# Kernel optimization log

Measured on AMD Instinct MI355X. Metric: run time of the kernel, lower is better.

The kernel has to match this reference:

```python
import jax, jax.numpy as jnp
import numpy as np

HEADS = 8
DIM_HEAD = 64


def setup_inputs() -> dict:
    key = jax.random.key(0)
    ks = jax.random.split(key, 5)
    B, N, C, coor = 2, 2048, 256, 3
    dim_inner = HEADS * DIM_HEAD  # 512
    # weight scale 1/16 ~ 1/sqrt(256) keeps softmax logits in a sane range
    w_scale = 1.0 / 16.0
    return {
        "x": jax.random.normal(ks[0], (B, N, C, coor), dtype=jnp.float32),
        "Wq": jax.random.normal(ks[1], (dim_inner, C), dtype=jnp.float32) * w_scale,
        "Wk": jax.random.normal(ks[2], (dim_inner, C), dtype=jnp.float32) * w_scale,
        "Wv": jax.random.normal(ks[3], (dim_inner, C), dtype=jnp.float32) * w_scale,
        "Wo": jax.random.normal(ks[4], (C, dim_inner), dtype=jnp.float32) * w_scale,
    }


def _split_heads(t, B, N, coor):
    # b n (h d) c -> b h n (d c)
    t = t.reshape(B, N, HEADS, DIM_HEAD, coor)
    t = t.transpose(0, 2, 1, 3, 4)
    return t.reshape(B, HEADS, N, DIM_HEAD * coor)


def reference(x, Wq, Wk, Wv, Wo):
    B, N, C, coor = x.shape
    # VNLinear: einsum('... i c, o i -> ... o c')
    q = jnp.einsum('bnic,oi->bnoc', x, Wq)
    k = jnp.einsum('bnic,oi->bnoc', x, Wk)
    v = jnp.einsum('bnic,oi->bnoc', x, Wv)
    q = _split_heads(q, B, N, coor)  # (B, H, N, d*c)
    k = _split_heads(k, B, N, coor)
    v = _split_heads(v, B, N, coor)
    scale = (DIM_HEAD * coor) ** -0.5
    sim = jnp.einsum('bhie,bhje->bhij', q, k) * scale  # (B, H, N, N)
    attn = jax.nn.softmax(sim, axis=-1)
    out = jnp.einsum('bhij,bhje->bhie', attn, v)  # (B, H, N, d*c)
    # b h n (d c) -> b n (h d) c
    out = out.reshape(B, HEADS, N, DIM_HEAD, coor).transpose(0, 2, 1, 3, 4)
    out = out.reshape(B, N, HEADS * DIM_HEAD, coor)
    # to_out VNLinear
    return jnp.einsum('bnic,oi->bnoc', out, Wo)  # (B, N, C, 3)
```

## Files before the change

kernel.cpp:

```cpp
#include <hip/hip_runtime.h>

#define HEADS 8
#define DH 64
#define CO 3
#define E 192
#define NSEQ 2048
#define BATCH 2
#define CIN 256
#define DINNER 512
#define NTOK 4096
#define BHTOT 16

typedef __attribute__((ext_vector_type(8))) short bf16x8;
typedef __attribute__((ext_vector_type(4))) short bf16x4;
typedef __attribute__((ext_vector_type(4))) float f32x4;

static __device__ inline short f2bf(float f) {
  union { float f; unsigned u; } v; v.f = f;
  unsigned r = (v.u + 0x7FFFu + ((v.u >> 16) & 1u)) >> 16;
  return (short)r;
}

static __device__ inline void load_lds16(const short* g, short* l) {
  __builtin_amdgcn_global_load_lds(
      (const __attribute__((address_space(1))) void*)g,
      (__attribute__((address_space(3))) void*)l, 16, 0, 0);
}


__global__ __launch_bounds__(256) void prep_w(const float* __restrict__ Wq,
                                              const float* __restrict__ Wk,
                                              const float* __restrict__ Wv,
                                              const float* __restrict__ Wo,
                                              short* __restrict__ wqkvp,
                                              short* __restrict__ wop) {
  int idx = blockIdx.x * 256 + threadIdx.x;
  const float qscale = 0.07216878364870323f * 1.4426950408889634f;
  if (idx < 1536 * 256) {
    int o = idx >> 8, i = idx & 255;
    float v;
    if (o < 512) v = Wq[idx] * qscale;
    else if (o < 1024) v = Wk[idx - 512 * 256];
    else v = Wv[idx - 1024 * 256];
    int nt = o >> 4, ln = o & 15, ks = i >> 5, qd = (i >> 3) & 3, j = i & 7;
    wqkvp[((size_t)(nt * 8 + ks)) * 512 + (qd * 16 + ln) * 8 + j] = f2bf(v);
  } else {
    int j0 = idx - 1536 * 256;
    if (j0 < 256 * 512) {
      int o2 = j0 >> 9, i = j0 & 511;
      int nt = o2 >> 4, ln = o2 & 15, ks = i >> 5, qd = (i >> 3) & 3, j = i & 7;
      wop[((size_t)(nt * 16 + ks)) * 512 + (qd * 16 + ln) * 8 + j] = f2bf(Wo[j0]);
    }
  }
}

__global__ __launch_bounds__(256) void prep_x(const float* __restrict__ x,
                                              short* __restrict__ xcp) {
  int idx = blockIdx.x * 256 + threadIdx.x;
  int t = idx >> 8, i = idx & 255;
  const float* p = x + (size_t)idx * 3;
  float a = p[0], b = p[1], c = p[2];
  int mt = t >> 4, ln = t & 15, ks = i >> 5, qd = (i >> 3) & 3, j = i & 7;
  size_t inner = (size_t)(qd * 16 + ln) * 8 + j;
  xcp[((size_t)(0 * 256 + mt) * 8 + ks) * 512 + inner] = f2bf(a);
  xcp[((size_t)(1 * 256 + mt) * 8 + ks) * 512 + inner] = f2bf(b);
  xcp[((size_t)(2 * 256 + mt) * 8 + ks) * 512 + inner] = f2bf(c);
}

__global__ __launch_bounds__(256) void qkv_gemm(const short* __restrict__ xcp,
                                                const short* __restrict__ wqkvp,
                                                short* __restrict__ qp,
                                                short* __restrict__ kp,
                                                short* __restrict__ vp) {
  __shared__ __align__(16) short pool[17408];
  int c = blockIdx.z, ntb = blockIdx.x, mtb = blockIdx.y;
  int tid = threadIdx.x, wave = tid >> 6, lane = tid & 63;
  int ln = lane & 15, quad = lane >> 4;
  int wm = wave >> 1, wn = wave & 1;

  const short* gA = xcp + ((size_t)(c * 256 + mtb * 8) * 8) * 512;
  const short* gB = wqkvp + ((size_t)(ntb * 8) * 8) * 512;

  f32x4 acc[4][4] = {};
#pragma unroll
  for (int i = 0; i < 2; i++) {
    int q = tid + 256 * i, mf = q >> 6, l = q & 63;
    load_lds16(gA + (size_t)(mf * 8) * 512 + l * 8, pool + q * 8);
    load_lds16(gB + (size_t)(mf * 8) * 512 + l * 8, pool + 8192 + q * 8);
  }
  for (int ks = 0; ks < 8; ks++) {
    int b = ks & 1;
    __syncthreads();
    if (ks < 7) {
#pragma unroll
      for (int i = 0; i < 2; i++) {
        int q = tid + 256 * i, mf = q >> 6, l = q & 63;
        load_lds16(gA + (size_t)(mf * 8 + ks + 1) * 512 + l * 8, pool + (b ^ 1) * 4096 + q * 8);
        load_lds16(gB + (size_t)(mf * 8 + ks + 1) * 512 + l * 8, pool + 8192 + (b ^ 1) * 4096 + q * 8);
      }
    }
    const short* As = pool + b * 4096;
    const short* Bs = pool + 8192 + b * 4096;
    bf16x8 af[4], bfr[4];
#pragma unroll
    for (int i = 0; i < 4; i++) af[i] = *(const bf16x8*)&As[(wm * 4 + i) * 512 + lane * 8];
#pragma unroll
    for (int j = 0; j < 4; j++) bfr[j] = *(const bf16x8*)&Bs[(wn * 4 + j) * 512 + lane * 8];
#pragma unroll
    for (int i = 0; i < 4; i++)
#pragma unroll
      for (int j = 0; j < 4; j++)
        acc[i][j] = __builtin_amdgcn_mfma_f32_16x16x32_bf16(af[i], bfr[j], acc[i][j], 0, 0, 0);
  }

  int mat = ntb >> 2;
  int b0 = mtb >> 4;
  if (mat < 2) {
    __syncthreads();
    short* tp = pool;
#pragma unroll
    for (int i = 0; i < 4; i++)
#pragma unroll
      for (int j = 0; j < 4; j++)
#pragma unroll
        for (int jj = 0; jj < 4; jj++)
          tp[(wm * 64 + i * 16 + quad * 4 + jj) * 136 + wn * 64 + j * 16 + ln] =
              f2bf(acc[i][j][jj]);
    __syncthreads();
    short* dst = (mat == 0) ? qp : kp;
    int h0 = (ntb & 3) * 2;
#pragma unroll
    for (int rep = 0; rep < 8; rep++) {
      int gi = rep * 256 + tid;
      int l2 = gi & 15, qd = (gi >> 4) & 3, nf2 = (gi >> 6) & 3,
          esp = (gi >> 8) & 1, hh = (gi >> 9) & 1, kt2 = gi >> 10;
      int tl = kt2 * 64 + nf2 * 16 + l2;
      bf16x8 val = *(const bf16x8*)&tp[tl * 136 + hh * 64 + (esp * 4 + qd) * 8];
      int bhx = b0 * 8 + h0 + hh;
      int kt = (mtb * 2 + kt2) & 31;
      int es = c * 2 + esp;
      size_t off = (((size_t)((bhx * 32 + kt) * 24) + es * 4 + nf2) * 64 +
                    (size_t)(qd * 16 + l2)) * 8;
      *(bf16x8*)(dst + off) = val;
    }
  } else {
#pragma unroll
    for (int i = 0; i < 4; i++) {
      int kt = (mtb * 2 + wm) & 31;
      int ks2 = (i >> 1) & 1;
      int qd2 = (i * 2 + (quad >> 1)) & 3;
#pragma unroll
      for (int j = 0; j < 4; j++) {
        int o = ntb * 128 + wn * 64 + j * 16 + ln;
        int oo = o & 511, h = oo >> 6, d = oo & 63;
        int ef = c * 4 + (d >> 4), l2v = d & 15;
        int bhx = b0 * 8 + h;
        size_t off = ((size_t)((bhx * 32 + kt) * 24 + ks2 * 12 + ef)) * 512 +
                     (qd2 * 16 + l2v) * 8 + (quad & 1) * 4;
        bf16x4 val = { f2bf(acc[i][j][0]), f2bf(acc[i][j][1]),
                       f2bf(acc[i][j][2]), f2bf(acc[i][j][3]) };
        *(bf16x4*)(vp + off) = val;
      }
    }
  }
}

__global__ __launch_bounds__(256, 2) void attn(const short* __restrict__ qp,
                                               const short* __restrict__ kp,
                                               const short* __restrict__ vp,
                                               short* __restrict__ opart,
                                               float* __restrict__ lpart) {
  __shared__ __align__(16) short pool[33792];
  int pair = blockIdx.x, qt = blockIdx.y;
  int bh = pair & 15, kh = pair >> 4;
  int tid = threadIdx.x, wave = tid >> 6, lane = tid & 63;
  int ln = lane & 15, quad = lane >> 4;
  short* Kl = pool;
  short* Vl = pool + 12288;
  short* Pl = pool + 24576;

  bf16x8 qf[2][6];
#pragma unroll
  for (int rg = 0; rg < 2; rg++) {
    int fi = wave * 2 + rg;
    const short* qb = qp +
        ((size_t)(bh * 32 + qt * 2 + (fi >> 2)) * 24 + (fi & 3)) * 512 + lane * 8;
#pragma unroll
    for (int es = 0; es < 6; es++) qf[rg][es] = *(const bf16x8*)(qb + es * 2048);
  }

  float l_r[2][4] = {};
  f32x4 acc[2][12] = {};
  const short* gKb = kp + (size_t)(bh * 32 + kh * 16) * 12288;
  const short* gVb = vp + (size_t)(bh * 32 + kh * 16) * 12288;

  for (int kt = 0; kt < 16; kt++) {
    const short* gK = gKb + (size_t)kt * 12288;
    const short* gV = gVb + (size_t)kt * 12288;
#pragma unroll
    for (int i = 0; i < 6; i++) {
      load_lds16(gK + (i * 256 + tid) * 8, Kl + (i * 256 + tid) * 8);
      load_lds16(gV + (i * 256 + tid) * 8, Vl + (i * 256 + tid) * 8);
    }
    __syncthreads();

    f32x4 s[2][4];
#pragma unroll
    for (int nf = 0; nf < 4; nf++) {
      f32x4 a0 = {}, a1 = {};
#pragma unroll
      for (int es = 0; es < 6; es++) {
        bf16x8 kf = *(const bf16x8*)&Kl[(es * 4 + nf) * 512 + lane * 8];
        a0 = __builtin_amdgcn_mfma_f32_16x16x32_bf16(qf[0][es], kf, a0, 0, 0, 0);
        a1 = __builtin_amdgcn_mfma_f32_16x16x32_bf16(qf[1][es], kf, a1, 0, 0, 0);
      }
      s[0][nf] = a0; s[1][nf] = a1;
    }

#pragma unroll
    for (int rg = 0; rg < 2; rg++)
#pragma unroll
      for (int jj = 0; jj < 4; jj++)
#pragma unroll
        for (int nf = 0; nf < 4; nf++) {
          float p = __builtin_amdgcn_exp2f(s[rg][nf][jj]);
          union { float f; unsigned u; } v; v.f = p;
          Pl[((wave * 2 + rg) * 16 + quad * 4 + jj) * 72 + nf * 16 + ln] =
              (short)((v.u + 0x8000u) >> 16);
          l_r[rg][jj] += p;
        }

    bf16x8 pa[2][2];
#pragma unroll
    for (int rg = 0; rg < 2; rg++) {
      const short* pb = &Pl[((wave * 2 + rg) * 16 + ln) * 72 + quad * 8];
      pa[rg][0] = *(const bf16x8*)pb;
      pa[rg][1] = *(const bf16x8*)(pb + 32);
    }
#pragma unroll
    for (int ef = 0; ef < 12; ef++) {
      bf16x8 v0 = *(const bf16x8*)&Vl[ef * 512 + lane * 8];
      bf16x8 v1 = *(const bf16x8*)&Vl[(12 + ef) * 512 + lane * 8];
#pragma unroll
      for (int rg = 0; rg < 2; rg++) {
        acc[rg][ef] = __builtin_amdgcn_mfma_f32_16x16x32_bf16(pa[rg][0], v0, acc[rg][ef], 0, 0, 0);
        acc[rg][ef] = __builtin_amdgcn_mfma_f32_16x16x32_bf16(pa[rg][1], v1, acc[rg][ef], 0, 0, 0);
      }
    }
    __syncthreads();
  }

#pragma unroll
  for (int rg = 0; rg < 2; rg++)
#pragma unroll
    for (int jj = 0; jj < 4; jj++)
#pragma unroll
      for (int off = 1; off < 16; off <<= 1)
        l_r[rg][jj] += __shfl_xor(l_r[rg][jj], off, 64);

  short* tp = pool;
#pragma unroll
  for (int rg = 0; rg < 2; rg++)
#pragma unroll
    for (int jj = 0; jj < 4; jj++) {
      int row = (wave * 2 + rg) * 16 + quad * 4 + jj;
#pragma unroll
      for (int ef = 0; ef < 12; ef++)
        tp[row * 200 + ef * 16 + ln] = f2bf(acc[rg][ef][jj]);
    }
  __syncthreads();
  const size_t obase = ((size_t)(kh * 16 + bh) * 2048 + qt * 128) * 192;
#pragma unroll
  for (int rep = 0; rep < 12; rep++) {
    int gi = rep * 256 + tid;
    int row = gi / 24, c8 = gi - row * 24;
    *(bf16x8*)(opart + obase + (size_t)row * 192 + c8 * 8) =
        *(const bf16x8*)&tp[row * 200 + c8 * 8];
  }
  int lb = (kh * 16 + bh) * 2048 + qt * 128;
  if (ln == 0) {
#pragma unroll
    for (int rg = 0; rg < 2; rg++)
#pragma unroll
      for (int jj = 0; jj < 4; jj++)
        lpart[lb + (wave * 2 + rg) * 16 + quad * 4 + jj] = l_r[rg][jj];
  }
}

__global__ __launch_bounds__(256) void merge(const short* __restrict__ opart,
                                             const float* __restrict__ lpart,
                                             short* __restrict__ owp) {
  int G = blockIdx.x * 256 + threadIdx.x;
  int inner = G & 63, qd = inner >> 4, row16 = inner & 15;
  int ks = (G >> 6) & 15, h = ks >> 1, esp = ks & 1;
  int mt = (G >> 10) & 255;
  int c = G >> 18;
  int t = mt * 16 + row16, b = t >> 11, n = t & 2047;
  int bh = b * 8 + h;
  size_t so = ((size_t)bh * 2048 + n) * 192 + c * 64 + esp * 32 + qd * 8;
  const size_t HSTR = (size_t)16 * 2048 * 192;
  bf16x8 o1 = *(const bf16x8*)(opart + so);
  bf16x8 o2 = *(const bf16x8*)(opart + HSTR + so);
  float l = lpart[bh * 2048 + n] + lpart[16 * 2048 + bh * 2048 + n];
  float inv = 1.f / l;
  bf16x8 r;
#pragma unroll
  for (int j = 0; j < 8; j++) {
    union { unsigned u; float f; } a, b2;
    a.u = ((unsigned)(unsigned short)o1[j]) << 16;
    b2.u = ((unsigned)(unsigned short)o2[j]) << 16;
    r[j] = f2bf((a.f + b2.f) * inv);
  }
  *(bf16x8*)(owp + (size_t)G * 8) = r;
}

__global__ __launch_bounds__(256) void out_gemm(const short* __restrict__ owp,
                                                const short* __restrict__ wop,
                                                float* __restrict__ out) {
  __shared__ __align__(16) short Al[4096], Bl[2048];
  int c = blockIdx.z, ntb = blockIdx.x, mtb = blockIdx.y;
  int tid = threadIdx.x, wave = tid >> 6, lane = tid & 63;
  int ln = lane & 15, quad = lane >> 4;
  int wm = wave >> 1, wn = wave & 1;

  f32x4 acc[4][2] = {};
  const short* gAb = owp + ((size_t)(c * 256 + mtb * 8) * 16) * 512;
  const short* gBb = wop + ((size_t)(ntb * 4) * 16) * 512;
  for (int ks = 0; ks < 16; ks++) {
#pragma unroll
    for (int i = 0; i < 2; i++) {
      int q = tid + 256 * i, mf = q >> 6, l = q & 63;
      load_lds16(gAb + (size_t)(mf * 16 + ks) * 512 + l * 8, &Al[q * 8]);
    }
    {
      int nf2 = tid >> 6;
      load_lds16(gBb + (size_t)(nf2 * 16 + ks) * 512 + lane * 8, &Bl[tid * 8]);
    }
    __syncthreads();
    bf16x8 af[4], bfr[2];
#pragma unroll
    for (int i = 0; i < 4; i++) af[i] = *(const bf16x8*)&Al[(wm * 4 + i) * 512 + lane * 8];
#pragma unroll
    for (int j = 0; j < 2; j++) bfr[j] = *(const bf16x8*)&Bl[(wn * 2 + j) * 512 + lane * 8];
#pragma unroll
    for (int i = 0; i < 4; i++)
#pragma unroll
      for (int j = 0; j < 2; j++)
        acc[i][j] = __builtin_amdgcn_mfma_f32_16x16x32_bf16(af[i], bfr[j], acc[i][j], 0, 0, 0);
    __syncthreads();
  }
#pragma unroll
  for (int i = 0; i < 4; i++) {
#pragma unroll
    for (int j = 0; j < 2; j++) {
      int o2 = ntb * 64 + (wn * 2 + j) * 16 + ln;
#pragma unroll
      for (int jj = 0; jj < 4; jj++) {
        int t = mtb * 128 + (wm * 4 + i) * 16 + quad * 4 + jj;
        out[((size_t)t * 256 + o2) * 3 + c] = acc[i][j][jj];
      }
    }
  }
}

extern "C" void kernel_launch(void* const* d_in, const int* in_sizes, int n_in,
                              void* d_out, int out_size, void* d_ws, size_t ws_size,
                              hipStream_t stream) {
  const float* x  = (const float*)d_in[0];
  const float* Wq = (const float*)d_in[1];
  const float* Wk = (const float*)d_in[2];
  const float* Wv = (const float*)d_in[3];
  const float* Wo = (const float*)d_in[4];
  float* out = (float*)d_out;

  short* ws    = (short*)d_ws;
  short* xcp   = ws;
  short* wqkvp = xcp + 3 * NTOK * CIN;
  short* wop   = wqkvp + 1536 * 256;
  short* qp    = wop + 256 * 512;
  short* kp    = qp + (size_t)BHTOT * NSEQ * E;
  short* vp    = kp + (size_t)BHTOT * NSEQ * E;
  short* owp   = vp + (size_t)BHTOT * NSEQ * E;
  short* opart = owp + (size_t)3 * NTOK * DINNER;
  float* lpart = (float*)(opart + (size_t)2 * BHTOT * NSEQ * E);

  prep_w<<<2048, 256, 0, stream>>>(Wq, Wk, Wv, Wo, wqkvp, wop);
  prep_x<<<NTOK * CIN / 256, 256, 0, stream>>>(x, xcp);
  qkv_gemm<<<dim3(12, 32, 3), 256, 0, stream>>>(xcp, wqkvp, qp, kp, vp);
  attn<<<dim3(32, 16), 256, 0, stream>>>(qp, kp, vp, opart, lpart);
  merge<<<3072, 256, 0, stream>>>(opart, lpart, owp);
  out_gemm<<<dim3(4, 32, 3), 256, 0, stream>>>(owp, wop, out);
}
```

Baseline: 173.6 us.

## Fuse split-KV merge into out_gemm A-tile load, add launch bounds

Removes the separate merge kernel and its round-trip through the owp buffer. out_gemm now reads both attention partials and a precomputed 1/l straight from global memory, sums and normalizes them, and writes bf16 into LDS. A tiny linv kernel precomputes the reciprocal of the summed softmax denominators. Min-blocks hints are added to qkv_gemm and out_gemm. In exchange, the out_gemm A loads become synchronous global loads with strided addressing instead of async global_load_lds, and each opart element is reread by every N-tile block (4x).

```diff
diff --git a/kernel.cpp b/kernel.cpp
--- a/kernel.cpp
+++ b/kernel.cpp
@@ -67,11 +67,11 @@
   xcp[((size_t)(2 * 256 + mt) * 8 + ks) * 512 + inner] = f2bf(c);
 }
 
-__global__ __launch_bounds__(256) void qkv_gemm(const short* __restrict__ xcp,
-                                                const short* __restrict__ wqkvp,
-                                                short* __restrict__ qp,
-                                                short* __restrict__ kp,
-                                                short* __restrict__ vp) {
+__global__ __launch_bounds__(256, 3) void qkv_gemm(const short* __restrict__ xcp,
+                                                   const short* __restrict__ wqkvp,
+                                                   short* __restrict__ qp,
+                                                   short* __restrict__ kp,
+                                                   short* __restrict__ vp) {
   __shared__ __align__(16) short pool[17408];
   int c = blockIdx.z, ntb = blockIdx.x, mtb = blockIdx.y;
   int tid = threadIdx.x, wave = tid >> 6, lane = tid & 63;
@@ -287,50 +287,45 @@
   }
 }
 
-__global__ __launch_bounds__(256) void merge(const short* __restrict__ opart,
-                                             const float* __restrict__ lpart,
-                                             short* __restrict__ owp) {
-  int G = blockIdx.x * 256 + threadIdx.x;
-  int inner = G & 63, qd = inner >> 4, row16 = inner & 15;
-  int ks = (G >> 6) & 15, h = ks >> 1, esp = ks & 1;
-  int mt = (G >> 10) & 255;
-  int c = G >> 18;
-  int t = mt * 16 + row16, b = t >> 11, n = t & 2047;
-  int bh = b * 8 + h;
-  size_t so = ((size_t)bh * 2048 + n) * 192 + c * 64 + esp * 32 + qd * 8;
-  const size_t HSTR = (size_t)16 * 2048 * 192;
-  bf16x8 o1 = *(const bf16x8*)(opart + so);
-  bf16x8 o2 = *(const bf16x8*)(opart + HSTR + so);
-  float l = lpart[bh * 2048 + n] + lpart[16 * 2048 + bh * 2048 + n];
-  float inv = 1.f / l;
-  bf16x8 r;
-#pragma unroll
-  for (int j = 0; j < 8; j++) {
-    union { unsigned u; float f; } a, b2;
-    a.u = ((unsigned)(unsigned short)o1[j]) << 16;
-    b2.u = ((unsigned)(unsigned short)o2[j]) << 16;
-    r[j] = f2bf((a.f + b2.f) * inv);
-  }
-  *(bf16x8*)(owp + (size_t)G * 8) = r;
-}
-
-__global__ __launch_bounds__(256) void out_gemm(const short* __restrict__ owp,
-                                                const short* __restrict__ wop,
-                                                float* __restrict__ out) {
+__global__ __launch_bounds__(256) void linv_k(const float* __restrict__ lpart,
+                                              float* __restrict__ linv) {
+  int i = blockIdx.x * 256 + threadIdx.x;
+  linv[i] = 1.f / (lpart[i] + lpart[32768 + i]);
+}
+
+__global__ __launch_bounds__(256, 2) void out_gemm(const short* __restrict__ opart,
+                                                   const float* __restrict__ linv,
+                                                   const short* __restrict__ wop,
+                                                   float* __restrict__ out) {
   __shared__ __align__(16) short Al[4096], Bl[2048];
   int c = blockIdx.z, ntb = blockIdx.x, mtb = blockIdx.y;
   int tid = threadIdx.x, wave = tid >> 6, lane = tid & 63;
   int ln = lane & 15, quad = lane >> 4;
   int wm = wave >> 1, wn = wave & 1;
+  const size_t HSTR = (size_t)16 * 2048 * 192;
 
   f32x4 acc[4][2] = {};
-  const short* gAb = owp + ((size_t)(c * 256 + mtb * 8) * 16) * 512;
   const short* gBb = wop + ((size_t)(ntb * 4) * 16) * 512;
   for (int ks = 0; ks < 16; ks++) {
 #pragma unroll
-    for (int i = 0; i < 2; i++) {
-      int q = tid + 256 * i, mf = q >> 6, l = q & 63;
-      load_lds16(gAb + (size_t)(mf * 16 + ks) * 512 + l * 8, &Al[q * 8]);
+    for (int ch = 0; ch < 2; ch++) {
+      int gi = ch * 256 + tid;
+      int mf = gi >> 6, qd = (gi >> 4) & 3, l2 = gi & 15;
+      int t = (mtb * 8 + mf) * 16 + l2;
+      int bh = (t >> 11) * 8 + (ks >> 1), n = t & 2047;
+      size_t base = ((size_t)bh * 2048 + n) * 192 + c * 64 + (ks & 1) * 32 + qd * 8;
+      bf16x8 o0 = *(const bf16x8*)(opart + base);
+      bf16x8 o1 = *(const bf16x8*)(opart + HSTR + base);
+      float iv = linv[bh * 2048 + n];
+      bf16x8 r;
+#pragma unroll
+      for (int j = 0; j < 8; j++) {
+        union { unsigned u; float f; } a, b;
+        a.u = ((unsigned)(unsigned short)o0[j]) << 16;
+        b.u = ((unsigned)(unsigned short)o1[j]) << 16;
+        r[j] = f2bf((a.f + b.f) * iv);
+      }
+      *(bf16x8*)&Al[mf * 512 + (qd * 16 + l2) * 8] = r;
     }
     {
       int nf2 = tid >> 6;
@@ -380,14 +375,15 @@
   short* qp    = wop + 256 * 512;
   short* kp    = qp + (size_t)BHTOT * NSEQ * E;
   short* vp    = kp + (size_t)BHTOT * NSEQ * E;
-  short* owp   = vp + (size_t)BHTOT * NSEQ * E;
-  short* opart = owp + (size_t)3 * NTOK * DINNER;
+  short* spare = vp + (size_t)BHTOT * NSEQ * E;
+  short* opart = spare + (size_t)3 * NTOK * DINNER;
   float* lpart = (float*)(opart + (size_t)2 * BHTOT * NSEQ * E);
+  float* linv  = (float*)spare;
 
   prep_w<<<2048, 256, 0, stream>>>(Wq, Wk, Wv, Wo, wqkvp, wop);
   prep_x<<<NTOK * CIN / 256, 256, 0, stream>>>(x, xcp);
   qkv_gemm<<<dim3(12, 32, 3), 256, 0, stream>>>(xcp, wqkvp, qp, kp, vp);
   attn<<<dim3(32, 16), 256, 0, stream>>>(qp, kp, vp, opart, lpart);
-  merge<<<3072, 256, 0, stream>>>(opart, lpart, owp);
-  out_gemm<<<dim3(4, 32, 3), 256, 0, stream>>>(owp, wop, out);
-}
+  linv_k<<<128, 256, 0, stream>>>(lpart, linv);
+  out_gemm<<<dim3(4, 32, 3), 256, 0, stream>>>(opart, linv, wop, out);
+}
```

Result: slower. 191.0 us (+10.0%).

## Split attention KV into three chunks and cut LDS and registers for occupancy

Applied to the files above, without the earlier changes.

The attention kernel now splits the key range into three chunks (11/11/10 tiles) instead of two, launching 768 blocks instead of 512 to better fill the GPU. It shrinks LDS by aliasing the P buffer onto the K buffer, which needs an extra barrier, and reloads Q fragments from global memory per tile instead of keeping them in registers. This lowers register and LDS pressure so three blocks fit per CU. The merge kernel sums three partials, and workspace buffers are aliased (lpart onto xcp, owp onto qp), which trades more global Q reloads and merge traffic for higher occupancy.

```diff
diff --git a/kernel.cpp b/kernel.cpp
--- a/kernel.cpp
+++ b/kernel.cpp
@@ -67,11 +67,11 @@
   xcp[((size_t)(2 * 256 + mt) * 8 + ks) * 512 + inner] = f2bf(c);
 }
 
-__global__ __launch_bounds__(256) void qkv_gemm(const short* __restrict__ xcp,
-                                                const short* __restrict__ wqkvp,
-                                                short* __restrict__ qp,
-                                                short* __restrict__ kp,
-                                                short* __restrict__ vp) {
+__global__ __launch_bounds__(256, 3) void qkv_gemm(const short* __restrict__ xcp,
+                                                   const short* __restrict__ wqkvp,
+                                                   short* __restrict__ qp,
+                                                   short* __restrict__ kp,
+                                                   short* __restrict__ vp) {
   __shared__ __align__(16) short pool[17408];
   int c = blockIdx.z, ntb = blockIdx.x, mtb = blockIdx.y;
   int tid = threadIdx.x, wave = tid >> 6, lane = tid & 63;
@@ -165,36 +165,34 @@
   }
 }
 
-__global__ __launch_bounds__(256, 2) void attn(const short* __restrict__ qp,
+__global__ __launch_bounds__(256, 3) void attn(const short* __restrict__ qp,
                                                const short* __restrict__ kp,
                                                const short* __restrict__ vp,
                                                short* __restrict__ opart,
                                                float* __restrict__ lpart) {
-  __shared__ __align__(16) short pool[33792];
+  __shared__ __align__(16) short pool[24576];
   int pair = blockIdx.x, qt = blockIdx.y;
-  int bh = pair & 15, kh = pair >> 4;
+  int bh = pair / 3, kh = pair - bh * 3;
   int tid = threadIdx.x, wave = tid >> 6, lane = tid & 63;
   int ln = lane & 15, quad = lane >> 4;
   short* Kl = pool;
   short* Vl = pool + 12288;
-  short* Pl = pool + 24576;
-
-  bf16x8 qf[2][6];
-#pragma unroll
-  for (int rg = 0; rg < 2; rg++) {
-    int fi = wave * 2 + rg;
-    const short* qb = qp +
-        ((size_t)(bh * 32 + qt * 2 + (fi >> 2)) * 24 + (fi & 3)) * 512 + lane * 8;
-#pragma unroll
-    for (int es = 0; es < 6; es++) qf[rg][es] = *(const bf16x8*)(qb + es * 2048);
-  }
+  short* Pl = pool;
+
+  int fi0 = wave * 2 + 0, fi1 = wave * 2 + 1;
+  const short* qb0 = qp +
+      ((size_t)(bh * 32 + qt * 2 + (fi0 >> 2)) * 24 + (fi0 & 3)) * 512 + lane * 8;
+  const short* qb1 = qp +
+      ((size_t)(bh * 32 + qt * 2 + (fi1 >> 2)) * 24 + (fi1 & 3)) * 512 + lane * 8;
 
   float l_r[2][4] = {};
   f32x4 acc[2][12] = {};
-  const short* gKb = kp + (size_t)(bh * 32 + kh * 16) * 12288;
-  const short* gVb = vp + (size_t)(bh * 32 + kh * 16) * 12288;
-
-  for (int kt = 0; kt < 16; kt++) {
+  int kt0 = kh * 11;
+  int ktn = (kh == 2) ? 10 : 11;
+  const short* gKb = kp + (size_t)(bh * 32 + kt0) * 12288;
+  const short* gVb = vp + (size_t)(bh * 32 + kt0) * 12288;
+
+  for (int kt = 0; kt < ktn; kt++) {
     const short* gK = gKb + (size_t)kt * 12288;
     const short* gV = gVb + (size_t)kt * 12288;
 #pragma unroll
@@ -204,31 +202,46 @@
     }
     __syncthreads();
 
-    f32x4 s[2][4];
-#pragma unroll
-    for (int nf = 0; nf < 4; nf++) {
-      f32x4 a0 = {}, a1 = {};
-#pragma unroll
-      for (int es = 0; es < 6; es++) {
+    f32x4 s[2][4] = {};
+#pragma unroll
+    for (int es = 0; es < 6; es++) {
+      bf16x8 q0 = *(const bf16x8*)(qb0 + es * 2048);
+      bf16x8 q1 = *(const bf16x8*)(qb1 + es * 2048);
+#pragma unroll
+      for (int nf = 0; nf < 4; nf++) {
         bf16x8 kf = *(const bf16x8*)&Kl[(es * 4 + nf) * 512 + lane * 8];
-        a0 = __builtin_amdgcn_mfma_f32_16x16x32_bf16(qf[0][es], kf, a0, 0, 0, 0);
-        a1 = __builtin_amdgcn_mfma_f32_16x16x32_bf16(qf[1][es], kf, a1, 0, 0, 0);
+        s[0][nf] = __builtin_amdgcn_mfma_f32_16x16x32_bf16(q0, kf, s[0][nf], 0, 0, 0);
+        s[1][nf] = __builtin_amdgcn_mfma_f32_16x16x32_bf16(q1, kf, s[1][nf], 0, 0, 0);
       }
-      s[0][nf] = a0; s[1][nf] = a1;
-    }
-
+    }
+
+    unsigned pk[2][4][2];
 #pragma unroll
     for (int rg = 0; rg < 2; rg++)
 #pragma unroll
-      for (int jj = 0; jj < 4; jj++)
-#pragma unroll
-        for (int nf = 0; nf < 4; nf++) {
-          float p = __builtin_amdgcn_exp2f(s[rg][nf][jj]);
-          union { float f; unsigned u; } v; v.f = p;
+      for (int nf = 0; nf < 4; nf++)
+#pragma unroll
+        for (int h2 = 0; h2 < 2; h2++) {
+          float pa = __builtin_amdgcn_exp2f(s[rg][nf][h2 * 2 + 0]);
+          float pb = __builtin_amdgcn_exp2f(s[rg][nf][h2 * 2 + 1]);
+          union { float f; unsigned u; } va, vb;
+          va.f = pa; vb.f = pb;
+          pk[rg][nf][h2] = ((va.u + 0x8000u) >> 16) |
+                           (((vb.u + 0x8000u) >> 16) << 16);
+          l_r[rg][h2 * 2 + 0] += pa;
+          l_r[rg][h2 * 2 + 1] += pb;
+        }
+
+    __syncthreads();
+
+#pragma unroll
+    for (int rg = 0; rg < 2; rg++)
+#pragma unroll
+      for (int nf = 0; nf < 4; nf++)
+#pragma unroll
+        for (int jj = 0; jj < 4; jj++)
           Pl[((wave * 2 + rg) * 16 + quad * 4 + jj) * 72 + nf * 16 + ln] =
-              (short)((v.u + 0x8000u) >> 16);
-          l_r[rg][jj] += p;
-        }
+              (short)(pk[rg][nf][jj >> 1] >> ((jj & 1) * 16));
 
     bf16x8 pa[2][2];
 #pragma unroll
@@ -266,7 +279,7 @@
       int row = (wave * 2 + rg) * 16 + quad * 4 + jj;
 #pragma unroll
       for (int ef = 0; ef < 12; ef++)
-        tp[row * 200 + ef * 16 + ln] = f2bf(acc[rg][ef][jj]);
+        tp[row * 192 + ef * 16 + ln] = f2bf(acc[rg][ef][jj]);
     }
   __syncthreads();
   const size_t obase = ((size_t)(kh * 16 + bh) * 2048 + qt * 128) * 192;
@@ -275,7 +288,7 @@
     int gi = rep * 256 + tid;
     int row = gi / 24, c8 = gi - row * 24;
     *(bf16x8*)(opart + obase + (size_t)row * 192 + c8 * 8) =
-        *(const bf16x8*)&tp[row * 200 + c8 * 8];
+        *(const bf16x8*)&tp[row * 192 + c8 * 8];
   }
   int lb = (kh * 16 + bh) * 2048 + qt * 128;
   if (ln == 0) {
@@ -291,26 +304,32 @@
                                              const float* __restrict__ lpart,
                                              short* __restrict__ owp) {
   int G = blockIdx.x * 256 + threadIdx.x;
-  int inner = G & 63, qd = inner >> 4, row16 = inner & 15;
+  int inner = G & 63;
   int ks = (G >> 6) & 15, h = ks >> 1, esp = ks & 1;
   int mt = (G >> 10) & 255;
   int c = G >> 18;
+  int row16 = inner & 15, qd = inner >> 4;
   int t = mt * 16 + row16, b = t >> 11, n = t & 2047;
   int bh = b * 8 + h;
   size_t so = ((size_t)bh * 2048 + n) * 192 + c * 64 + esp * 32 + qd * 8;
   const size_t HSTR = (size_t)16 * 2048 * 192;
-  bf16x8 o1 = *(const bf16x8*)(opart + so);
-  bf16x8 o2 = *(const bf16x8*)(opart + HSTR + so);
-  float l = lpart[bh * 2048 + n] + lpart[16 * 2048 + bh * 2048 + n];
+  float acc[8] = {};
+  float l = 0.f;
+#pragma unroll
+  for (int khp = 0; khp < 3; khp++) {
+    bf16x8 o = *(const bf16x8*)(opart + khp * HSTR + so);
+#pragma unroll
+    for (int j = 0; j < 8; j++) {
+      union { unsigned u; float f; } a;
+      a.u = ((unsigned)(unsigned short)o[j]) << 16;
+      acc[j] += a.f;
+    }
+    l += lpart[khp * 16 * 2048 + bh * 2048 + n];
+  }
   float inv = 1.f / l;
   bf16x8 r;
 #pragma unroll
-  for (int j = 0; j < 8; j++) {
-    union { unsigned u; float f; } a, b2;
-    a.u = ((unsigned)(unsigned short)o1[j]) << 16;
-    b2.u = ((unsigned)(unsigned short)o2[j]) << 16;
-    r[j] = f2bf((a.f + b2.f) * inv);
-  }
+  for (int j = 0; j < 8; j++) r[j] = f2bf(acc[j] * inv);
   *(bf16x8*)(owp + (size_t)G * 8) = r;
 }
 
@@ -380,14 +399,14 @@
   short* qp    = wop + 256 * 512;
   short* kp    = qp + (size_t)BHTOT * NSEQ * E;
   short* vp    = kp + (size_t)BHTOT * NSEQ * E;
-  short* owp   = vp + (size_t)BHTOT * NSEQ * E;
-  short* opart = owp + (size_t)3 * NTOK * DINNER;
-  float* lpart = (float*)(opart + (size_t)2 * BHTOT * NSEQ * E);
+  short* opart = vp + (size_t)BHTOT * NSEQ * E;
+  float* lpart = (float*)xcp;
+  short* owp   = qp;
 
   prep_w<<<2048, 256, 0, stream>>>(Wq, Wk, Wv, Wo, wqkvp, wop);
   prep_x<<<NTOK * CIN / 256, 256, 0, stream>>>(x, xcp);
   qkv_gemm<<<dim3(12, 32, 3), 256, 0, stream>>>(xcp, wqkvp, qp, kp, vp);
-  attn<<<dim3(32, 16), 256, 0, stream>>>(qp, kp, vp, opart, lpart);
+  attn<<<dim3(48, 16), 256, 0, stream>>>(qp, kp, vp, opart, lpart);
   merge<<<3072, 256, 0, stream>>>(opart, lpart, owp);
   out_gemm<<<dim3(4, 32, 3), 256, 0, stream>>>(owp, wop, out);
 }
```

After: 208.4 us. 1.2x slower.
